# Performance work log

Hardware: AMD Instinct MI355X
Metric: run time of the kernel (lower is better)

Reference implementation:

```python
import jax, jax.numpy as jnp
import numpy as np

D, C, H, W = 8, 512, 64, 64


def setup_inputs() -> dict:
    key = jax.random.key(0)
    k1, k2, k3 = jax.random.split(key, 3)
    x = jax.random.normal(k1, (D, C, H, W), dtype=jnp.float32)
    atten = jax.random.normal(k2, (D, C, C), dtype=jnp.float32)
    gamma = jax.random.normal(k3, (1,), dtype=jnp.float32)
    return {"x": x, "atten": atten, "gamma": gamma}


def reference(x, atten, gamma):
    d, c, h, w = x.shape
    q = x.reshape(d, c, h * w)              # q == v == flattened x; k = q^T
    # energy[d, i, j] = <channel_i, channel_j> over spatial positions
    energy = jnp.einsum('din,djn->dij', q, q)
    # max-centering: rowmax - energy (note the sign flip vs standard softmax)
    energy_new = jnp.max(energy, axis=-1, keepdims=True) - energy
    attention = jax.nn.softmax(energy_new, axis=-1)
    attention = jax.nn.softmax(attention + atten, axis=-1)
    # out = attention^T @ v : out[d, j, n] = sum_i attention[d, i, j] * v[d, i, n]
    out = jnp.einsum('dij,din->djn', attention, q).reshape(d, c, h, w)
    return gamma * out + x
```

## Files before the change

kernel.cpp:

```cpp
#include <hip/hip_runtime.h>
#include <hip/hip_bf16.h>

#define DD 8
#define CC 512
#define NN 4096

typedef __bf16 bf16x8 __attribute__((ext_vector_type(8)));
typedef float  f32x4  __attribute__((ext_vector_type(4)));
typedef ushort ush8   __attribute__((ext_vector_type(8)));

__device__ __forceinline__ ushort f2bf(float f) {
  unsigned u = __float_as_uint(f);
  u = (u + 0x7fffu + ((u >> 16) & 1u)) >> 16;
  return (ushort)u;
}
__device__ __forceinline__ float bf2f(ushort h) {
  return __uint_as_float(((unsigned)h) << 16);
}

__device__ __forceinline__ void gl_lds16(const ushort* g, ushort* l) {
  __builtin_amdgcn_global_load_lds(
      (const __attribute__((address_space(1))) void*)g,
      (__attribute__((address_space(3))) void*)l, 16, 0, 0);
}


__global__ __launch_bounds__(256) void k0_convert(
    const float* __restrict__ x, ushort* __restrict__ qh,
    ushort* __restrict__ ql, ushort* __restrict__ qt) {
  int d = blockIdx.z, ct = blockIdx.y, nt = blockIdx.x;
  __shared__ ushort T[64][68];
  int t = threadIdx.x;
  int rr = t >> 4;
  int c4 = (t & 15) * 4;
  const float* xb = x + ((size_t)(d * CC + ct * 64)) * NN + nt * 64;
#pragma unroll
  for (int it = 0; it < 4; ++it) {
    int r = it * 16 + rr;
    float4 v = *(const float4*)(xb + (size_t)r * NN + c4);
    ushort h0 = f2bf(v.x), h1 = f2bf(v.y), h2 = f2bf(v.z), h3 = f2bf(v.w);
    ushort l0 = f2bf(v.x - bf2f(h0)), l1 = f2bf(v.y - bf2f(h1));
    ushort l2 = f2bf(v.z - bf2f(h2)), l3 = f2bf(v.w - bf2f(h3));
    size_t qi = ((size_t)(d * CC + ct * 64 + r)) * NN + nt * 64 + c4;
    *(ushort4*)(qh + qi) = make_ushort4(h0, h1, h2, h3);
    *(ushort4*)(ql + qi) = make_ushort4(l0, l1, l2, l3);
    *(ushort4*)&T[r][c4] = make_ushort4(h0, h1, h2, h3);
  }
  __syncthreads();
#pragma unroll
  for (int it = 0; it < 4; ++it) {
    int nl = it * 16 + rr;
    ushort4 v = make_ushort4(T[c4 + 0][nl], T[c4 + 1][nl], T[c4 + 2][nl], T[c4 + 3][nl]);
    *(ushort4*)(qt + ((size_t)(d * NN + nt * 64 + nl)) * CC + ct * 64 + c4) = v;
  }
}

#define K1_STAGE(S)                                                            \
  {                                                                            \
    ushort* ls = lbase + ((S) & 1) * 8192;                                     \
    const ushort* gs = gsrc + (size_t)(S) * 32;                                \
    _Pragma("unroll")                                                          \
    for (int c = 0; c < 8; ++c)                                                \
      gl_lds16(gs + (size_t)c * 16 * NN, ls + c * 512);                        \
  }

#define K1_COMPUTE(SOFF)                                                       \
  {                                                                            \
    bf16x8 ah[4], al[4];                                                       \
    _Pragma("unroll")                                                          \
    for (int mi = 0; mi < 4; ++mi) {                                           \
      int off = (SOFF) + (wm + mi * 16 + fr) * 32 + qo;                        \
      ah[mi] = *(const bf16x8*)&As[off];                                       \
      al[mi] = *(const bf16x8*)&As[off + 4096];                                \
    }                                                                          \
    _Pragma("unroll")                                                          \
    for (int ni = 0; ni < 4; ++ni) {                                           \
      int off = (SOFF) + (wn + ni * 16 + fr) * 32 + qo;                        \
      bf16x8 bh = *(const bf16x8*)&Bs[off];                                    \
      bf16x8 bl = *(const bf16x8*)&Bs[off + 4096];                             \
      _Pragma("unroll")                                                        \
      for (int mi = 0; mi < 4; ++mi) {                                         \
        acc[mi][ni] = __builtin_amdgcn_mfma_f32_16x16x32_bf16(ah[mi], bh, acc[mi][ni], 0, 0, 0); \
        acc[mi][ni] = __builtin_amdgcn_mfma_f32_16x16x32_bf16(ah[mi], bl, acc[mi][ni], 0, 0, 0); \
        acc[mi][ni] = __builtin_amdgcn_mfma_f32_16x16x32_bf16(al[mi], bh, acc[mi][ni], 0, 0, 0); \
      }                                                                        \
    }                                                                          \
  }

__global__ __launch_bounds__(256, 2) void k1_gram(
    const ushort* __restrict__ qh, const ushort* __restrict__ ql,
    float* __restrict__ Ep, int ns, int nkk, int ksp) {
  __shared__ ushort As[2 * 2 * 4096];
  __shared__ ushort Bs[2 * 2 * 4096];
  int b = blockIdx.x;
  int s = b % ns;
  int rem = b / ns;
  int tile = rem % 10, d = rem / 10;
  int tm = (int)((0x3221110000ULL >> (tile * 4)) & 15ULL);
  int tn = (int)((0x3323213210ULL >> (tile * 4)) & 15ULL);
  int t = threadIdx.x, lane = t & 63, w = t >> 6;
  int wm = (w >> 1) * 64, wn = (w & 1) * 64;
  int qd = lane >> 4, fr = lane & 15;
  int qo = (qd ^ ((fr >> 1) & 3)) * 8;
  int so = ((lane & 3) ^ ((lane >> 3) & 3)) * 8;

  const ushort* srcbase = (w & 1) ? ql : qh;
  int rowblk = (w < 2) ? tm : tn;
  const ushort* gsrc = srcbase +
      ((size_t)(d * CC + rowblk * 128 + (lane >> 2))) * NN +
      (size_t)s * ksp + so;
  ushort* lbase = ((w < 2) ? As : Bs) + (w & 1) * 4096;

  f32x4 acc[4][4];
#pragma unroll
  for (int i = 0; i < 4; ++i)
#pragma unroll
    for (int j = 0; j < 4; ++j) acc[i][j] = (f32x4){0.f, 0.f, 0.f, 0.f};

  K1_STAGE(0)

#pragma unroll 1
  for (int kk = 0; kk < nkk - 1; ++kk) {
    asm volatile("s_waitcnt lgkmcnt(0)\n\ts_barrier" ::: "memory");
    K1_STAGE(kk + 1)
    asm volatile("s_waitcnt vmcnt(8)\n\ts_barrier" ::: "memory");
    K1_COMPUTE((kk & 1) * 8192)
  }
  asm volatile("s_waitcnt vmcnt(0) lgkmcnt(0)\n\ts_barrier" ::: "memory");
  K1_COMPUTE(((nkk - 1) & 1) * 8192)

  size_t ebase = ((size_t)(s * DD + d)) * ((size_t)CC * CC);
#pragma unroll
  for (int mi = 0; mi < 4; ++mi) {
    int r0 = tm * 128 + wm + mi * 16 + qd * 4;
#pragma unroll
    for (int ni = 0; ni < 4; ++ni) {
      int c0 = tn * 128 + wn + ni * 16 + fr;
      float* ep = Ep + ebase + (size_t)r0 * CC + c0;
#pragma unroll
      for (int r = 0; r < 4; ++r) ep[(size_t)r * CC] = acc[mi][ni][r];
    }
  }
  if (tm != tn) {
#pragma unroll
    for (int mi = 0; mi < 4; ++mi) {
      int r0 = tm * 128 + wm + mi * 16 + qd * 4;
#pragma unroll
      for (int ni = 0; ni < 4; ++ni) {
        int c0 = tn * 128 + wn + ni * 16 + fr;
        float4 v = make_float4(acc[mi][ni][0], acc[mi][ni][1],
                               acc[mi][ni][2], acc[mi][ni][3]);
        *(float4*)(Ep + ebase + (size_t)c0 * CC + r0) = v;
      }
    }
  }
}

__device__ __forceinline__ float wmin(float v) {
#pragma unroll
  for (int o = 32; o > 0; o >>= 1) v = fminf(v, __shfl_xor(v, o));
  return v;
}
__device__ __forceinline__ float wmax(float v) {
#pragma unroll
  for (int o = 32; o > 0; o >>= 1) v = fmaxf(v, __shfl_xor(v, o));
  return v;
}
__device__ __forceinline__ float wsum(float v) {
#pragma unroll
  for (int o = 32; o > 0; o >>= 1) v += __shfl_xor(v, o);
  return v;
}

__global__ __launch_bounds__(256) void k2_softmax(
    const float* __restrict__ Ep, const float* __restrict__ atten,
    ushort* __restrict__ a2t, int ns) {
  int d = blockIdx.x & 7;
  int i0 = (blockIdx.x >> 3) * 8;
  int t = threadIdx.x, lane = t & 63, w = t >> 6;
  int j8 = lane * 8;
  __shared__ ushort T[8][520];
  const size_t SP = (size_t)DD * CC * CC;

#pragma unroll
  for (int r2 = 0; r2 < 2; ++r2) {
    int ri = w * 2 + r2;
    size_t base = ((size_t)(d * CC + i0 + ri)) * CC + j8;
    f32x4 a0 = (f32x4){0.f, 0.f, 0.f, 0.f};
    f32x4 a1 = (f32x4){0.f, 0.f, 0.f, 0.f};
    for (int s = 0; s < ns; ++s) {
      const float* p = Ep + (size_t)s * SP + base;
      a0 += *(const f32x4*)p;
      a1 += *(const f32x4*)(p + 4);
    }
    float mn = fminf(fminf(fminf(a0[0], a0[1]), fminf(a0[2], a0[3])),
                     fminf(fminf(a1[0], a1[1]), fminf(a1[2], a1[3])));
    mn = wmin(mn);
    float p0 = __expf(mn - a0[0]), p1 = __expf(mn - a0[1]);
    float p2 = __expf(mn - a0[2]), p3 = __expf(mn - a0[3]);
    float p4 = __expf(mn - a1[0]), p5 = __expf(mn - a1[1]);
    float p6 = __expf(mn - a1[2]), p7 = __expf(mn - a1[3]);
    float s1 = wsum(p0 + p1 + p2 + p3 + p4 + p5 + p6 + p7);
    float inv1 = 1.0f / s1;
    const float* ap = atten + base;
    f32x4 t0 = *(const f32x4*)ap;
    f32x4 t1 = *(const f32x4*)(ap + 4);
    float u0 = p0 * inv1 + t0[0], u1 = p1 * inv1 + t0[1];
    float u2 = p2 * inv1 + t0[2], u3 = p3 * inv1 + t0[3];
    float u4 = p4 * inv1 + t1[0], u5 = p5 * inv1 + t1[1];
    float u6 = p6 * inv1 + t1[2], u7 = p7 * inv1 + t1[3];
    float mx = wmax(fmaxf(fmaxf(fmaxf(u0, u1), fmaxf(u2, u3)),
                          fmaxf(fmaxf(u4, u5), fmaxf(u6, u7))));
    float q0 = __expf(u0 - mx), q1 = __expf(u1 - mx);
    float q2 = __expf(u2 - mx), q3 = __expf(u3 - mx);
    float q4 = __expf(u4 - mx), q5 = __expf(u5 - mx);
    float q6 = __expf(u6 - mx), q7 = __expf(u7 - mx);
    float s2 = wsum(q0 + q1 + q2 + q3 + q4 + q5 + q6 + q7);
    float inv2 = 1.0f / s2;
    ush8 o;
    o[0] = f2bf(q0 * inv2); o[1] = f2bf(q1 * inv2);
    o[2] = f2bf(q2 * inv2); o[3] = f2bf(q3 * inv2);
    o[4] = f2bf(q4 * inv2); o[5] = f2bf(q5 * inv2);
    o[6] = f2bf(q6 * inv2); o[7] = f2bf(q7 * inv2);
    *(ush8*)&T[ri][j8] = o;
  }
  __syncthreads();
#pragma unroll
  for (int it = 0; it < 2; ++it) {
    int j = t + it * 256;
    ush8 o;
#pragma unroll
    for (int k = 0; k < 8; ++k) o[k] = T[k][j];
    *(ush8*)&a2t[((size_t)(d * CC + j)) * CC + i0] = o;
  }
}

#define K3_COMPUTE(SOFF)                                                       \
  {                                                                            \
    bf16x8 qf[4];                                                              \
    _Pragma("unroll")                                                          \
    for (int ii = 0; ii < 4; ++ii)                                             \
      qf[ii] = *(const bf16x8*)&Bs[(SOFF) + (wn2 + ii * 16 + fr) * 32 + qo];   \
    _Pragma("unroll")                                                          \
    for (int jj = 0; jj < 4; ++jj) {                                           \
      bf16x8 af = *(const bf16x8*)&As[(SOFF) + (wj + jj * 16 + fr) * 32 + qo]; \
      _Pragma("unroll")                                                        \
      for (int ii = 0; ii < 4; ++ii)                                           \
        acc[ii][jj] = __builtin_amdgcn_mfma_f32_16x16x32_bf16(                 \
            qf[ii], af, acc[ii][jj], 0, 0, 0);                                 \
    }                                                                          \
  }

#define K3_STAGE(S)                                                            \
  {                                                                            \
    ushort* ls = mylds + ((S) & 3) * 4096;                                     \
    const ushort* gs = g0 + (size_t)(S) * 32;                                  \
    _Pragma("unroll")                                                          \
    for (int c = 0; c < 4; ++c)                                                \
      gl_lds16(gs + (size_t)(c * 16) * CC, ls + c * 512);                      \
  }

__global__ __launch_bounds__(256, 2) void k3_out(
    const ushort* __restrict__ a2t, const ushort* __restrict__ qt,
    const float* __restrict__ x, const float* __restrict__ gamma,
    float* __restrict__ out) {
  __shared__ ushort As[4 * 128 * 32];
  __shared__ ushort Bs[4 * 128 * 32];
  int b = blockIdx.x;
  int d = b & 7;
  int nt = (b >> 3) & 31, jt = b >> 8;
  int t = threadIdx.x, lane = t & 63, w = t >> 6;
  int wj = (w >> 1) * 64, wn2 = (w & 1) * 64;
  int qd = lane >> 4, fr = lane & 15;
  int qo = (qd ^ ((fr >> 1) & 3)) * 8;
  int so = ((lane & 3) ^ ((lane >> 3) & 3)) * 8;

  const ushort* src = (w < 2)
      ? (a2t + (size_t)d * CC * CC + (size_t)(jt * 128) * CC)
      : (qt + (size_t)d * NN * CC + (size_t)(nt * 128) * CC);
  int cbase = (w & 1) * 4;
  const ushort* g0 = src + ((size_t)(cbase * 16 + (lane >> 2))) * CC + so;
  ushort* mylds = ((w < 2) ? As : Bs) + cbase * 512;

  f32x4 acc[4][4];
#pragma unroll
  for (int i = 0; i < 4; ++i)
#pragma unroll
    for (int j = 0; j < 4; ++j) acc[i][j] = (f32x4){0.f, 0.f, 0.f, 0.f};

  K3_STAGE(0)
  K3_STAGE(1)
  K3_STAGE(2)

#pragma unroll 1
  for (int kk = 0; kk < 13; ++kk) {
    asm volatile("s_waitcnt vmcnt(8)\n\ts_barrier" ::: "memory");
    K3_STAGE(kk + 3)
    K3_COMPUTE((kk & 3) * 4096)
  }
  asm volatile("s_waitcnt vmcnt(8)\n\ts_barrier" ::: "memory");
  K3_COMPUTE(1 * 4096)
  asm volatile("s_waitcnt vmcnt(4)\n\ts_barrier" ::: "memory");
  K3_COMPUTE(2 * 4096)
  asm volatile("s_waitcnt vmcnt(0)\n\ts_barrier" ::: "memory");

  int n0b = nt * 128 + wn2 + qd * 4;
  float4 xp0[4], xp1[4];
#pragma unroll
  for (int jj = 0; jj < 4; ++jj) {
    size_t rb = ((size_t)(d * CC + jt * 128 + wj + jj * 16 + fr)) * NN;
    xp0[jj] = *(const float4*)(x + rb + n0b);
    xp1[jj] = *(const float4*)(x + rb + n0b + 16);
  }
  K3_COMPUTE(3 * 4096)

  float g = gamma[0];
  float4 x2[4], x3[4];
#pragma unroll
  for (int jj = 0; jj < 4; ++jj)
    x2[jj] = *(const float4*)(x + ((size_t)(d * CC + jt * 128 + wj + jj * 16 + fr)) * NN + n0b + 32);
#pragma unroll
  for (int jj = 0; jj < 4; ++jj) {
    size_t idx = ((size_t)(d * CC + jt * 128 + wj + jj * 16 + fr)) * NN + n0b;
    *(float4*)(out + idx) = make_float4(g * acc[0][jj][0] + xp0[jj].x,
                                        g * acc[0][jj][1] + xp0[jj].y,
                                        g * acc[0][jj][2] + xp0[jj].z,
                                        g * acc[0][jj][3] + xp0[jj].w);
  }
#pragma unroll
  for (int jj = 0; jj < 4; ++jj)
    x3[jj] = *(const float4*)(x + ((size_t)(d * CC + jt * 128 + wj + jj * 16 + fr)) * NN + n0b + 48);
#pragma unroll
  for (int jj = 0; jj < 4; ++jj) {
    size_t idx = ((size_t)(d * CC + jt * 128 + wj + jj * 16 + fr)) * NN + n0b + 16;
    *(float4*)(out + idx) = make_float4(g * acc[1][jj][0] + xp1[jj].x,
                                        g * acc[1][jj][1] + xp1[jj].y,
                                        g * acc[1][jj][2] + xp1[jj].z,
                                        g * acc[1][jj][3] + xp1[jj].w);
  }
#pragma unroll
  for (int jj = 0; jj < 4; ++jj) {
    size_t idx = ((size_t)(d * CC + jt * 128 + wj + jj * 16 + fr)) * NN + n0b + 32;
    *(float4*)(out + idx) = make_float4(g * acc[2][jj][0] + x2[jj].x,
                                        g * acc[2][jj][1] + x2[jj].y,
                                        g * acc[2][jj][2] + x2[jj].z,
                                        g * acc[2][jj][3] + x2[jj].w);
  }
#pragma unroll
  for (int jj = 0; jj < 4; ++jj) {
    size_t idx = ((size_t)(d * CC + jt * 128 + wj + jj * 16 + fr)) * NN + n0b + 48;
    *(float4*)(out + idx) = make_float4(g * acc[3][jj][0] + x3[jj].x,
                                        g * acc[3][jj][1] + x3[jj].y,
                                        g * acc[3][jj][2] + x3[jj].z,
                                        g * acc[3][jj][3] + x3[jj].w);
  }
}

extern "C" void kernel_launch(void* const* d_in, const int* in_sizes, int n_in,
                              void* d_out, int out_size, void* d_ws, size_t ws_size,
                              hipStream_t stream) {
  (void)in_sizes; (void)n_in; (void)out_size;
  const float* x     = (const float*)d_in[0];
  const float* atten = (const float*)d_in[1];
  const float* gamma = (const float*)d_in[2];
  float* out = (float*)d_out;

  char* ws = (char*)d_ws;
  ushort* qh  = (ushort*)(ws);
  ushort* ql  = (ushort*)(ws + 33554432);
  ushort* qt  = (ushort*)(ws + 67108864);
  ushort* a2t = (ushort*)(ws + 100663296);
  float*  Ep  = (float*) (ws + 104857600);

  int ns = (ws_size >= 104857600ULL + 8ULL * 8388608ULL) ? 8 : 4;
  int ksp = NN / ns;
  int nkk = ksp / 32;

  k0_convert<<<dim3(64, 8, 8), 256, 0, stream>>>(x, qh, ql, qt);
  k1_gram   <<<dim3(80 * ns), 256, 0, stream>>>(qh, ql, Ep, ns, nkk, ksp);
  k2_softmax<<<dim3(512), 256, 0, stream>>>(Ep, atten, a2t, ns);
  k3_out    <<<dim3(1024), 256, 0, stream>>>(a2t, qt, x, gamma, out);
}
```

Before: 228.8 us.

## Enlarge k3 output tile to 128x256 and skip duplicate B staging on diagonal gram tiles

```diff
diff --git a/kernel.cpp b/kernel.cpp
--- a/kernel.cpp
+++ b/kernel.cpp
@@ -76,8 +76,8 @@
     _Pragma("unroll")                                                          \
     for (int ni = 0; ni < 4; ++ni) {                                           \
       int off = (SOFF) + (wn + ni * 16 + fr) * 32 + qo;                        \
-      bf16x8 bh = *(const bf16x8*)&Bs[off];                                    \
-      bf16x8 bl = *(const bf16x8*)&Bs[off + 4096];                             \
+      bf16x8 bh = *(const bf16x8*)&Bp[off];                                    \
+      bf16x8 bl = *(const bf16x8*)&Bp[off + 4096];                             \
       _Pragma("unroll")                                                        \
       for (int mi = 0; mi < 4; ++mi) {                                         \
         acc[mi][ni] = __builtin_amdgcn_mfma_f32_16x16x32_bf16(ah[mi], bh, acc[mi][ni], 0, 0, 0); \
@@ -104,6 +104,10 @@
   int qo = (qd ^ ((fr >> 1) & 3)) * 8;
   int so = ((lane & 3) ^ ((lane >> 3) & 3)) * 8;
 
+  int diag = (tm == tn);
+  const ushort* Bp = diag ? As : Bs;
+  int doStage = (w < 2) || !diag;
+
   const ushort* srcbase = (w & 1) ? ql : qh;
   int rowblk = (w < 2) ? tm : tn;
   const ushort* gsrc = srcbase +
@@ -117,12 +121,12 @@
 #pragma unroll
     for (int j = 0; j < 4; ++j) acc[i][j] = (f32x4){0.f, 0.f, 0.f, 0.f};
 
-  K1_STAGE(0)
+  if (doStage) K1_STAGE(0)
 
 #pragma unroll 1
   for (int kk = 0; kk < nkk - 1; ++kk) {
     asm volatile("s_waitcnt lgkmcnt(0)\n\ts_barrier" ::: "memory");
-    K1_STAGE(kk + 1)
+    if (doStage) K1_STAGE(kk + 1)
     asm volatile("s_waitcnt vmcnt(8)\n\ts_barrier" ::: "memory");
     K1_COMPUTE((kk & 1) * 8192)
   }
@@ -141,7 +145,7 @@
       for (int r = 0; r < 4; ++r) ep[(size_t)r * CC] = acc[mi][ni][r];
     }
   }
-  if (tm != tn) {
+  if (!diag) {
 #pragma unroll
     for (int mi = 0; mi < 4; ++mi) {
       int r0 = tm * 128 + wm + mi * 16 + qd * 4;
@@ -235,124 +239,124 @@
   }
 }
 
-#define K3_COMPUTE(SOFF)                                                       \
-  {                                                                            \
-    bf16x8 qf[4];                                                              \
-    _Pragma("unroll")                                                          \
-    for (int ii = 0; ii < 4; ++ii)                                             \
-      qf[ii] = *(const bf16x8*)&Bs[(SOFF) + (wn2 + ii * 16 + fr) * 32 + qo];   \
+#define K3_STAGE(S)                                                            \
+  {                                                                            \
+    ushort* ls = lds0 + ((S) % 3) * stsz;                                      \
+    const ushort* gs = g0 + (size_t)(S) * 32;                                  \
+    _Pragma("unroll")                                                          \
+    for (int c = 0; c < 4; ++c)                                                \
+      gl_lds16(gs + (size_t)(c * 16) * CC, ls + c * 512);                      \
+    if (!isA) {                                                                \
+      _Pragma("unroll")                                                        \
+      for (int c = 4; c < 8; ++c)                                              \
+        gl_lds16(gs + (size_t)(c * 16) * CC, ls + c * 512);                    \
+    }                                                                          \
+  }
+
+#define K3_COMPUTE(S)                                                          \
+  {                                                                            \
+    int soA = ((S) % 3) * 4096, soB = ((S) % 3) * 8192;                        \
+    bf16x8 qf[8];                                                              \
+    _Pragma("unroll")                                                          \
+    for (int ii = 0; ii < 8; ++ii)                                             \
+      qf[ii] = *(const bf16x8*)&Bs[soB + (wn2 + ii * 16 + fr) * 32 + qo];      \
     _Pragma("unroll")                                                          \
     for (int jj = 0; jj < 4; ++jj) {                                           \
-      bf16x8 af = *(const bf16x8*)&As[(SOFF) + (wj + jj * 16 + fr) * 32 + qo]; \
+      bf16x8 af = *(const bf16x8*)&As[soA + (wj + jj * 16 + fr) * 32 + qo];    \
       _Pragma("unroll")                                                        \
-      for (int ii = 0; ii < 4; ++ii)                                           \
+      for (int ii = 0; ii < 8; ++ii)                                           \
         acc[ii][jj] = __builtin_amdgcn_mfma_f32_16x16x32_bf16(                 \
             qf[ii], af, acc[ii][jj], 0, 0, 0);                                 \
     }                                                                          \
   }
 
-#define K3_STAGE(S)                                                            \
-  {                                                                            \
-    ushort* ls = mylds + ((S) & 3) * 4096;                                     \
-    const ushort* gs = g0 + (size_t)(S) * 32;                                  \
-    _Pragma("unroll")                                                          \
-    for (int c = 0; c < 4; ++c)                                                \
-      gl_lds16(gs + (size_t)(c * 16) * CC, ls + c * 512);                      \
+#define K3_WAIT                                                                \
+  {                                                                            \
+    if (isA) asm volatile("s_waitcnt vmcnt(4)" ::: "memory");                  \
+    else     asm volatile("s_waitcnt vmcnt(8)" ::: "memory");                  \
+    asm volatile("s_barrier" ::: "memory");                                    \
   }
 
 __global__ __launch_bounds__(256, 2) void k3_out(
     const ushort* __restrict__ a2t, const ushort* __restrict__ qt,
     const float* __restrict__ x, const float* __restrict__ gamma,
     float* __restrict__ out) {
-  __shared__ ushort As[4 * 128 * 32];
-  __shared__ ushort Bs[4 * 128 * 32];
+  __shared__ ushort As[3 * 4096];
+  __shared__ ushort Bs[3 * 8192];
   int b = blockIdx.x;
-  int d = b & 7;
-  int nt = (b >> 3) & 31, jt = b >> 8;
+  int d = b >> 6, ntp = (b >> 2) & 15, jt = b & 3;
   int t = threadIdx.x, lane = t & 63, w = t >> 6;
-  int wj = (w >> 1) * 64, wn2 = (w & 1) * 64;
+  int wj = (w >> 1) * 64;
+  int wn2 = (w & 1) * 128;
   int qd = lane >> 4, fr = lane & 15;
   int qo = (qd ^ ((fr >> 1) & 3)) * 8;
   int so = ((lane & 3) ^ ((lane >> 3) & 3)) * 8;
 
-  const ushort* src = (w < 2)
+  int isA = (w < 2);
+  const ushort* src = isA
       ? (a2t + (size_t)d * CC * CC + (size_t)(jt * 128) * CC)
-      : (qt + (size_t)d * NN * CC + (size_t)(nt * 128) * CC);
-  int cbase = (w & 1) * 4;
-  const ushort* g0 = src + ((size_t)(cbase * 16 + (lane >> 2))) * CC + so;
-  ushort* mylds = ((w < 2) ? As : Bs) + cbase * 512;
-
-  f32x4 acc[4][4];
-#pragma unroll
-  for (int i = 0; i < 4; ++i)
+      : (qt + (size_t)d * NN * CC + (size_t)(ntp * 256) * CC);
+  int rbase = (w & 1) * (isA ? 64 : 128);
+  const ushort* g0 = src + ((size_t)(rbase + (lane >> 2))) * CC + so;
+  ushort* lds0 = (isA ? As : Bs) + rbase * 32;
+  int stsz = isA ? 4096 : 8192;
+
+  f32x4 acc[8][4];
+#pragma unroll
+  for (int i = 0; i < 8; ++i)
 #pragma unroll
     for (int j = 0; j < 4; ++j) acc[i][j] = (f32x4){0.f, 0.f, 0.f, 0.f};
 
   K3_STAGE(0)
   K3_STAGE(1)
-  K3_STAGE(2)
 
 #pragma unroll 1
-  for (int kk = 0; kk < 13; ++kk) {
-    asm volatile("s_waitcnt vmcnt(8)\n\ts_barrier" ::: "memory");
-    K3_STAGE(kk + 3)
-    K3_COMPUTE((kk & 3) * 4096)
-  }
-  asm volatile("s_waitcnt vmcnt(8)\n\ts_barrier" ::: "memory");
-  K3_COMPUTE(1 * 4096)
-  asm volatile("s_waitcnt vmcnt(4)\n\ts_barrier" ::: "memory");
-  K3_COMPUTE(2 * 4096)
-  asm volatile("s_waitcnt vmcnt(0)\n\ts_barrier" ::: "memory");
-
-  int n0b = nt * 128 + wn2 + qd * 4;
-  float4 xp0[4], xp1[4];
+  for (int kk = 0; kk < 14; ++kk) {
+    K3_WAIT
+    K3_STAGE(kk + 2)
+    K3_COMPUTE(kk)
+  }
+  K3_WAIT
+  K3_COMPUTE(14)
+  asm volatile("s_waitcnt vmcnt(0)" ::: "memory");
+  asm volatile("s_barrier" ::: "memory");
+
+  float g = gamma[0];
+  int n0b = ntp * 256 + wn2 + qd * 4;
+  int jb = jt * 128 + wj + fr;
+  float4 xp[4], xq[4];
 #pragma unroll
   for (int jj = 0; jj < 4; ++jj) {
-    size_t rb = ((size_t)(d * CC + jt * 128 + wj + jj * 16 + fr)) * NN;
-    xp0[jj] = *(const float4*)(x + rb + n0b);
-    xp1[jj] = *(const float4*)(x + rb + n0b + 16);
-  }
-  K3_COMPUTE(3 * 4096)
-
-  float g = gamma[0];
-  float4 x2[4], x3[4];
-#pragma unroll
-  for (int jj = 0; jj < 4; ++jj)
-    x2[jj] = *(const float4*)(x + ((size_t)(d * CC + jt * 128 + wj + jj * 16 + fr)) * NN + n0b + 32);
-#pragma unroll
-  for (int jj = 0; jj < 4; ++jj) {
-    size_t idx = ((size_t)(d * CC + jt * 128 + wj + jj * 16 + fr)) * NN + n0b;
-    *(float4*)(out + idx) = make_float4(g * acc[0][jj][0] + xp0[jj].x,
-                                        g * acc[0][jj][1] + xp0[jj].y,
-                                        g * acc[0][jj][2] + xp0[jj].z,
-                                        g * acc[0][jj][3] + xp0[jj].w);
-  }
-#pragma unroll
-  for (int jj = 0; jj < 4; ++jj)
-    x3[jj] = *(const float4*)(x + ((size_t)(d * CC + jt * 128 + wj + jj * 16 + fr)) * NN + n0b + 48);
-#pragma unroll
-  for (int jj = 0; jj < 4; ++jj) {
-    size_t idx = ((size_t)(d * CC + jt * 128 + wj + jj * 16 + fr)) * NN + n0b + 16;
-    *(float4*)(out + idx) = make_float4(g * acc[1][jj][0] + xp1[jj].x,
-                                        g * acc[1][jj][1] + xp1[jj].y,
-                                        g * acc[1][jj][2] + xp1[jj].z,
-                                        g * acc[1][jj][3] + xp1[jj].w);
-  }
-#pragma unroll
-  for (int jj = 0; jj < 4; ++jj) {
-    size_t idx = ((size_t)(d * CC + jt * 128 + wj + jj * 16 + fr)) * NN + n0b + 32;
-    *(float4*)(out + idx) = make_float4(g * acc[2][jj][0] + x2[jj].x,
-                                        g * acc[2][jj][1] + x2[jj].y,
-                                        g * acc[2][jj][2] + x2[jj].z,
-                                        g * acc[2][jj][3] + x2[jj].w);
-  }
-#pragma unroll
-  for (int jj = 0; jj < 4; ++jj) {
-    size_t idx = ((size_t)(d * CC + jt * 128 + wj + jj * 16 + fr)) * NN + n0b + 48;
-    *(float4*)(out + idx) = make_float4(g * acc[3][jj][0] + x3[jj].x,
-                                        g * acc[3][jj][1] + x3[jj].y,
-                                        g * acc[3][jj][2] + x3[jj].z,
-                                        g * acc[3][jj][3] + x3[jj].w);
+    size_t rb = ((size_t)(d * CC + jb + jj * 16)) * NN;
+    xp[jj] = *(const float4*)(x + rb + n0b);
+    xq[jj] = *(const float4*)(x + rb + n0b + 16);
+  }
+  K3_COMPUTE(15)
+
+#pragma unroll
+  for (int ii = 0; ii < 8; ++ii) {
+    float4 xn[4];
+    if (ii < 6) {
+#pragma unroll
+      for (int jj = 0; jj < 4; ++jj)
+        xn[jj] = *(const float4*)(x + ((size_t)(d * CC + jb + jj * 16)) * NN +
+                                  n0b + (ii + 2) * 16);
+    }
+#pragma unroll
+    for (int jj = 0; jj < 4; ++jj) {
+      size_t idx = ((size_t)(d * CC + jb + jj * 16)) * NN + n0b + ii * 16;
+      *(float4*)(out + idx) = make_float4(g * acc[ii][jj][0] + xp[jj].x,
+                                          g * acc[ii][jj][1] + xp[jj].y,
+                                          g * acc[ii][jj][2] + xp[jj].z,
+                                          g * acc[ii][jj][3] + xp[jj].w);
+    }
+    if (ii < 6) {
+#pragma unroll
+      for (int jj = 0; jj < 4; ++jj) { xp[jj] = xq[jj]; xq[jj] = xn[jj]; }
+    } else if (ii == 6) {
+#pragma unroll
+      for (int jj = 0; jj < 4; ++jj) xp[jj] = xq[jj];
+    }
   }
 }
 
@@ -379,5 +383,5 @@
   k0_convert<<<dim3(64, 8, 8), 256, 0, stream>>>(x, qh, ql, qt);
   k1_gram   <<<dim3(80 * ns), 256, 0, stream>>>(qh, ql, Ep, ns, nkk, ksp);
   k2_softmax<<<dim3(512), 256, 0, stream>>>(Ep, atten, a2t, ns);
-  k3_out    <<<dim3(1024), 256, 0, stream>>>(a2t, qt, x, gamma, out);
-}
+  k3_out    <<<dim3(512), 256, 0, stream>>>(a2t, qt, x, gamma, out);
+}
```

After: 243.2 us. 1.06x slower.
